# Kernel optimization log

Measured on AMD Instinct MI355X. Metric: run time of the kernel, lower is better.

## Reference

```python
import jax, jax.numpy as jnp
import numpy as np

B, T, C, H = 4, 2048, 768, 12
D = C // H  # head dim = 64

def setup_inputs() -> dict:
    key = jax.random.key(0)
    k1, k2, k3 = jax.random.split(key, 3)
    x = jax.random.normal(k1, (B, T, C), dtype=jnp.float32)
    W_attn = jax.random.normal(k2, (C, 3 * C), dtype=jnp.float32) * 0.02
    b_attn = jnp.zeros((3 * C,), dtype=jnp.float32)
    W_proj = jax.random.normal(k3, (C, C), dtype=jnp.float32) * 0.02
    b_proj = jnp.zeros((C,), dtype=jnp.float32)
    return {"x": x, "W_attn": W_attn, "b_attn": b_attn, "W_proj": W_proj, "b_proj": b_proj}

def reference(x, W_attn, b_attn, W_proj, b_proj):
    Bx, Tx, Cx = x.shape
    qkv = x @ W_attn + b_attn                      # [B,T,3C]
    q, k, v = jnp.split(qkv, 3, axis=2)
    q = q.reshape(Bx, Tx, H, D).swapaxes(1, 2)     # [B,H,T,D]
    k = k.reshape(Bx, Tx, H, D).swapaxes(1, 2)
    v = v.reshape(Bx, Tx, H, D).swapaxes(1, 2)
    att = jnp.einsum('bhqd,bhkd->bhqk', q, k) / jnp.sqrt(jnp.float32(D))
    mask = jnp.tril(jnp.ones((Tx, Tx), dtype=bool))
    att = jnp.where(mask, att, -jnp.inf)
    att = jax.nn.softmax(att, axis=-1)
    y = jnp.einsum('bhqk,bhkd->bhqd', att, v)      # [B,H,T,D]
    y = y.swapaxes(1, 2).reshape(Bx, Tx, Cx)
    return y @ W_proj + b_proj
```

## Files before the change

### kernel.cpp

```cpp
#include <hip/hip_runtime.h>
#include <hip/hip_bf16.h>

#define BATCH 4
#define TSEQ  2048
#define CDIM  768
#define HNUM  12
#define DHEAD 64
#define NQKV  (3*CDIM)
#define BTOT  (BATCH*TSEQ)
#define BH    (BATCH*HNUM)

typedef unsigned short u16;
typedef __attribute__((ext_vector_type(8))) __bf16 bf16x8;
typedef __attribute__((ext_vector_type(4))) float f32x4;

#define MFMA16(a,b,c) __builtin_amdgcn_mfma_f32_16x16x32_bf16((a),(b),(c),0,0,0)

__device__ __forceinline__ u16 f2b(float f) {
    union { float f; unsigned u; } v; v.f = f;
    unsigned u = v.u;
    unsigned r = (u + 0x7fffu + ((u >> 16) & 1u)) >> 16;
    return (u16)r;
}

__device__ __forceinline__ unsigned cvtpk(float lo, float hi) {
    unsigned r;
    asm("v_cvt_pk_bf16_f32 %0, %1, %2" : "=v"(r) : "v"(lo), "v"(hi));
    return r;
}

__device__ __forceinline__ float fexp2(float x) {
    float r;
    asm("v_exp_f32 %0, %1" : "=v"(r) : "v"(x));
    return r;
}

__device__ __forceinline__ void gload_lds(const void* g, void* l) {
    __builtin_amdgcn_global_load_lds(
        (const __attribute__((address_space(1))) void*)g,
        (__attribute__((address_space(3))) void*)l, 16, 0, 0);
}

__global__ __launch_bounds__(256) void cast_f32_bf16(
        const float* __restrict__ in, u16* __restrict__ out, int n4) {
    int i = blockIdx.x * blockDim.x + threadIdx.x;
    if (i >= n4) return;
    float4 a = reinterpret_cast<const float4*>(in)[i];
    ushort4 o;
    o.x = f2b(a.x); o.y = f2b(a.y); o.z = f2b(a.z); o.w = f2b(a.w);
    reinterpret_cast<ushort4*>(out)[i] = o;
}

__global__ __launch_bounds__(256) void tcast(
        const float* __restrict__ in, u16* __restrict__ out, int R, int Cc) {
    __shared__ float tile[32][33];
    int c0 = blockIdx.x * 32, r0 = blockIdx.y * 32;
    int tx = threadIdx.x, ty = threadIdx.y;
    #pragma unroll
    for (int i = 0; i < 32; i += 8)
        tile[ty + i][tx] = in[(size_t)(r0 + ty + i) * Cc + c0 + tx];
    __syncthreads();
    #pragma unroll
    for (int i = 0; i < 32; i += 8)
        out[(size_t)(c0 + ty + i) * R + r0 + tx] = f2b(tile[tx][ty + i]);
}

template<int NX>
__global__ __launch_bounds__(256, 2) void gemm_qkv(
        const u16* __restrict__ A, const u16* __restrict__ Bt,
        const float* __restrict__ bias,
        u16* __restrict__ qb, u16* __restrict__ kb, u16* __restrict__ vtb,
        int K) {
    __shared__ u16 sA[3][128 * 32];
    __shared__ u16 sB[3][256 * 32];
    const int tid = threadIdx.x;
    const int lane = tid & 63;
    const int w = tid >> 6;
    const int g = lane >> 4, lr = lane & 15;
    const int cpx = gridDim.x >> 3;
    const int wg = ((int)blockIdx.x & 7) * cpx + ((int)blockIdx.x >> 3);
    const int bx = wg % NX, by = wg / NX;
    const int m0 = by * 128, n0 = bx * 256;

    f32x4 acc[8][4] = {};

    auto stage = [&](int buf, int kt) {
        #pragma unroll
        for (int i = 0; i < 2; ++i) {
            int c = i * 256 + tid, r = c >> 2, s = c & 3;
            int c8 = s ^ ((r >> 1) & 3);
            gload_lds(A + (size_t)(m0 + r) * K + kt * 32 + c8 * 8, &sA[buf][c * 8]);
        }
        #pragma unroll
        for (int i = 0; i < 4; ++i) {
            int c = i * 256 + tid, r = c >> 2, s = c & 3;
            int c8 = s ^ ((r >> 1) & 3);
            gload_lds(Bt + (size_t)(n0 + r) * K + kt * 32 + c8 * 8, &sB[buf][c * 8]);
        }
    };

    const int KT = K / 32;
    stage(0, 0); stage(1, 1);
    for (int kt = 0; kt < KT; ++kt) {
        if (kt + 1 < KT) asm volatile("s_waitcnt vmcnt(6)" ::: "memory");
        else             asm volatile("s_waitcnt vmcnt(0)" ::: "memory");
        __builtin_amdgcn_s_barrier();
        if (kt + 2 < KT) stage((kt + 2) % 3, kt + 2);
        const u16* cA = sA[kt % 3];
        const u16* cB = sB[kt % 3];
        bf16x8 af[8], bfr[4];
        #pragma unroll
        for (int m = 0; m < 8; ++m) {
            int r = m * 16 + lr;
            af[m] = *(const bf16x8*)&cA[r * 32 + ((g ^ ((r >> 1) & 3)) << 3)];
        }
        #pragma unroll
        for (int n = 0; n < 4; ++n) {
            int r = w * 64 + n * 16 + lr;
            bfr[n] = *(const bf16x8*)&cB[r * 32 + ((g ^ ((r >> 1) & 3)) << 3)];
        }
        __builtin_amdgcn_s_setprio(1);
        #pragma unroll
        for (int m = 0; m < 8; ++m)
            #pragma unroll
            for (int n = 0; n < 4; ++n)
                acc[m][n] = MFMA16(bfr[n], af[m], acc[m][n]);
        __builtin_amdgcn_s_setprio(0);
    }

    const int which = n0 / CDIM;
    #pragma unroll
    for (int m = 0; m < 8; ++m) {
        const int rg = m0 + m * 16 + lr;
        const int b = rg >> 11, t = rg & (TSEQ - 1);
        #pragma unroll
        for (int n = 0; n < 4; ++n) {
            const int cg = n0 + w * 64 + n * 16 + (g << 2);
            const int c  = cg - which * CDIM;
            const int h  = c >> 6, d = c & 63;
            const size_t bh = (size_t)(b * HNUM + h);
            const float4 bv = *(const float4*)&bias[cg];
            const float v0 = acc[m][n][0] + bv.x;
            const float v1 = acc[m][n][1] + bv.y;
            const float v2 = acc[m][n][2] + bv.z;
            const float v3 = acc[m][n][3] + bv.w;
            if (which == 0) {
                const float s = 0.1803368801111243f;
                ushort4 pv;
                pv.x = f2b(v0 * s); pv.y = f2b(v1 * s);
                pv.z = f2b(v2 * s); pv.w = f2b(v3 * s);
                *(ushort4*)&qb[(bh * TSEQ + t) * DHEAD + d] = pv;
            } else if (which == 1) {
                ushort4 pv;
                pv.x = f2b(v0); pv.y = f2b(v1); pv.z = f2b(v2); pv.w = f2b(v3);
                *(ushort4*)&kb[(bh * TSEQ + t) * DHEAD + d] = pv;
            } else {
                vtb[(bh * DHEAD + d + 0) * TSEQ + t] = f2b(v0);
                vtb[(bh * DHEAD + d + 1) * TSEQ + t] = f2b(v1);
                vtb[(bh * DHEAD + d + 2) * TSEQ + t] = f2b(v2);
                vtb[(bh * DHEAD + d + 3) * TSEQ + t] = f2b(v3);
            }
        }
    }
}

template<int NX>
__global__ __launch_bounds__(256) void gemm_out(
        const u16* __restrict__ A, const u16* __restrict__ Bt,
        const float* __restrict__ bias, float* __restrict__ outf, int K) {
    __shared__ u16 sA[3][128 * 32];
    __shared__ u16 sB[3][128 * 32];
    const int tid = threadIdx.x;
    const int lane = tid & 63;
    const int w = tid >> 6;
    const int wr = w >> 1, wc = w & 1;
    const int cpx = gridDim.x >> 3;
    const int wg = ((int)blockIdx.x & 7) * cpx + ((int)blockIdx.x >> 3);
    const int bx = wg % NX, by = wg / NX;
    const int m0 = by * 128, n0 = bx * 128;

    f32x4 acc[4][4] = {};

    auto stage = [&](int buf, int kt) {
        #pragma unroll
        for (int i = 0; i < 2; ++i) {
            int chunk = i * 256 + tid;
            int row = chunk >> 2, c8 = chunk & 3;
            gload_lds(A  + (size_t)(m0 + row) * K + kt * 32 + c8 * 8, &sA[buf][chunk * 8]);
            gload_lds(Bt + (size_t)(n0 + row) * K + kt * 32 + c8 * 8, &sB[buf][chunk * 8]);
        }
    };

    const int KT = K / 32;
    stage(0, 0); stage(1, 1);
    for (int kt = 0; kt < KT; ++kt) {
        if (kt + 1 < KT) asm volatile("s_waitcnt vmcnt(4)" ::: "memory");
        else             asm volatile("s_waitcnt vmcnt(0)" ::: "memory");
        __builtin_amdgcn_s_barrier();
        if (kt + 2 < KT) stage((kt + 2) % 3, kt + 2);
        const u16* cA = sA[kt % 3];
        const u16* cB = sB[kt % 3];
        bf16x8 af[4], bfr[4];
        #pragma unroll
        for (int m = 0; m < 4; ++m)
            af[m] = *(const bf16x8*)&cA[(wr * 64 + m * 16 + (lane & 15)) * 32 + ((lane >> 4) << 3)];
        #pragma unroll
        for (int n = 0; n < 4; ++n)
            bfr[n] = *(const bf16x8*)&cB[(wc * 64 + n * 16 + (lane & 15)) * 32 + ((lane >> 4) << 3)];
        #pragma unroll
        for (int m = 0; m < 4; ++m)
            #pragma unroll
            for (int n = 0; n < 4; ++n)
                acc[m][n] = MFMA16(bfr[n], af[m], acc[m][n]);
    }

    #pragma unroll
    for (int m = 0; m < 4; ++m) {
        const int rg = m0 + wr * 64 + m * 16 + (lane & 15);
        #pragma unroll
        for (int n = 0; n < 4; ++n) {
            const int cg = n0 + wc * 64 + n * 16 + ((lane >> 4) << 2);
            const float4 bv = *(const float4*)&bias[cg];
            float4 ov;
            ov.x = acc[m][n][0] + bv.x;
            ov.y = acc[m][n][1] + bv.y;
            ov.z = acc[m][n][2] + bv.z;
            ov.w = acc[m][n][3] + bv.w;
            *(float4*)&outf[(size_t)rg * CDIM + cg] = ov;
        }
    }
}

__global__ __launch_bounds__(256, 4) void attn_fwd(
        const u16* __restrict__ qb, const u16* __restrict__ kb,
        const u16* __restrict__ vtb, u16* __restrict__ yb) {
    __shared__ u16 sK[2][64 * 64];
    __shared__ u16 sVt[2][64 * 64];
    const int qt = 31 - (int)(blockIdx.x / BH);
    const int bh = blockIdx.x % BH;
    const int b = bh / HNUM, h = bh % HNUM;
    const int tid = threadIdx.x, lane = tid & 63, w = tid >> 6;
    const int g = lane >> 4, lq = lane & 15;
    const int qlo = qt * 64 + w * 16;
    const u16* qbase = qb  + (size_t)bh * TSEQ * DHEAD;
    const u16* kbase = kb  + (size_t)bh * TSEQ * DHEAD;
    const u16* vbase = vtb + (size_t)bh * DHEAD * TSEQ;

    bf16x8 qf[2];
    #pragma unroll
    for (int ks = 0; ks < 2; ++ks)
        qf[ks] = *(const bf16x8*)&qbase[(size_t)(qlo + lq) * DHEAD + ks * 32 + g * 8];

    union { unsigned u[4]; bf16x8 v; } ones;
    #pragma unroll
    for (int i = 0; i < 4; ++i) ones.u[i] = 0x3f803f80u;

    f32x4 o[4] = {};
    f32x4 ls = {};
    float mx = -__builtin_inff();

    auto STAGE = [&](int buf, int kt) {
        const int k0 = kt << 6;
        #pragma unroll
        for (int i = 0; i < 2; ++i) {
            int chunk = i * 256 + tid;
            int srow = chunk >> 3;
            int cb = ((chunk & 7) << 4) ^ ((srow & 7) << 4);
            gload_lds(kbase + (size_t)(k0 + srow) * DHEAD + (cb >> 1), &sK[buf][chunk * 8]);
            gload_lds(vbase + (size_t)srow * TSEQ + k0 + (cb >> 1),    &sVt[buf][chunk * 8]);
        }
    };

    const int nk = qt + 1;
    STAGE(0, 0);
    __syncthreads();
    for (int kt = 0; kt < nk; ++kt) {
        const int k0 = kt << 6;
        if (kt + 1 < nk) STAGE((kt + 1) & 1, kt + 1);
        const u16* cK = sK[kt & 1];
        const u16* cV = sVt[kt & 1];
        f32x4 s[4];
        #pragma unroll
        for (int n = 0; n < 4; ++n) s[n] = f32x4{0.f, 0.f, 0.f, 0.f};
        __builtin_amdgcn_s_setprio(1);
        #pragma unroll
        for (int n = 0; n < 4; ++n) {
            #pragma unroll
            for (int ks = 0; ks < 2; ++ks) {
                int r = n * 16 + lq;
                int lb = (r * 128 + (ks * 32 + g * 8) * 2) ^ ((r & 7) << 4);
                bf16x8 kf = *(const bf16x8*)((const char*)cK + lb);
                s[n] = MFMA16(kf, qf[ks], s[n]);
            }
        }
        __builtin_amdgcn_s_setprio(0);
        if (k0 + 63 > qlo) {
            const int qa = qlo + lq;
            #pragma unroll
            for (int n = 0; n < 4; ++n)
                #pragma unroll
                for (int j = 0; j < 4; ++j)
                    if (k0 + n * 16 + g * 4 + j > qa) s[n][j] = -__builtin_inff();
        }
        float t0 = fmaxf(fmaxf(s[0][0], s[0][1]), fmaxf(s[0][2], s[0][3]));
        float t1 = fmaxf(fmaxf(s[1][0], s[1][1]), fmaxf(s[1][2], s[1][3]));
        float t2 = fmaxf(fmaxf(s[2][0], s[2][1]), fmaxf(s[2][2], s[2][3]));
        float t3 = fmaxf(fmaxf(s[3][0], s[3][1]), fmaxf(s[3][2], s[3][3]));
        float tmax = fmaxf(fmaxf(t0, t1), fmaxf(t2, t3));
        tmax = fmaxf(tmax, __shfl_xor(tmax, 16));
        tmax = fmaxf(tmax, __shfl_xor(tmax, 32));
        if (__any(tmax > mx + 8.0f)) {
            float mnew = fmaxf(mx, tmax);
            float sc = fexp2(mx - mnew);
            mx = mnew;
            #pragma unroll
            for (int j = 0; j < 4; ++j) {
                float scj = __shfl(sc, (lane & 48) | ((g << 2) + j));
                ls[j] *= scj;
                #pragma unroll
                for (int n = 0; n < 4; ++n) o[n][j] *= scj;
            }
        }
        #pragma unroll
        for (int n = 0; n < 4; ++n)
            #pragma unroll
            for (int j = 0; j < 4; ++j)
                s[n][j] = fexp2(s[n][j] - mx);
        unsigned apk[4], bpk[4];
        #pragma unroll
        for (int n = 0; n < 4; ++n) {
            apk[n] = cvtpk(s[n][0], s[n][1]);
            bpk[n] = cvtpk(s[n][2], s[n][3]);
        }
        const int s0l = lq + ((lane & 16) << 1);
        const bool hi = (lane & 32) != 0;
        #pragma unroll
        for (int ks = 0; ks < 2; ++ks) {
            unsigned A0  = (unsigned)__shfl((int)apk[2 * ks],     s0l);
            unsigned B0  = (unsigned)__shfl((int)bpk[2 * ks],     s0l);
            unsigned A1  = (unsigned)__shfl((int)apk[2 * ks + 1], s0l);
            unsigned B1  = (unsigned)__shfl((int)bpk[2 * ks + 1], s0l);
            unsigned A0h = (unsigned)__shfl((int)apk[2 * ks],     s0l + 16);
            unsigned B0h = (unsigned)__shfl((int)bpk[2 * ks],     s0l + 16);
            unsigned A1h = (unsigned)__shfl((int)apk[2 * ks + 1], s0l + 16);
            unsigned B1h = (unsigned)__shfl((int)bpk[2 * ks + 1], s0l + 16);
            union { unsigned u[4]; bf16x8 v; } pa;
            pa.u[0] = hi ? A1  : A0;
            pa.u[1] = hi ? B1  : B0;
            pa.u[2] = hi ? A1h : A0h;
            pa.u[3] = hi ? B1h : B0h;
            __builtin_amdgcn_s_setprio(1);
            #pragma unroll
            for (int n = 0; n < 4; ++n) {
                int d = n * 16 + lq;
                int lb = (d * 128 + (ks * 32 + g * 8) * 2) ^ ((d & 7) << 4);
                bf16x8 vf = *(const bf16x8*)((const char*)cV + lb);
                o[n] = MFMA16(pa.v, vf, o[n]);
            }
            ls = MFMA16(pa.v, ones.v, ls);
            __builtin_amdgcn_s_setprio(0);
        }
        __syncthreads();
    }

    #pragma unroll
    for (int j = 0; j < 4; ++j) {
        float inv = 1.f / ls[j];
        const int t = qlo + g * 4 + j;
        #pragma unroll
        for (int n = 0; n < 4; ++n) {
            const int c = h * DHEAD + n * 16 + lq;
            yb[((size_t)b * TSEQ + t) * CDIM + c] = f2b(o[n][j] * inv);
        }
    }
}

extern "C" void kernel_launch(void* const* d_in, const int* in_sizes, int n_in,
                              void* d_out, int out_size, void* d_ws, size_t ws_size,
                              hipStream_t stream) {
    const float* x      = (const float*)d_in[0];
    const float* W_attn = (const float*)d_in[1];
    const float* b_attn = (const float*)d_in[2];
    const float* W_proj = (const float*)d_in[3];
    const float* b_proj = (const float*)d_in[4];
    float* out = (float*)d_out;

    u16* ws = (u16*)d_ws;
    u16* xb     = ws;
    u16* yb     = xb;
    u16* WattnT = xb     + (size_t)BTOT * CDIM;
    u16* WprojT = WattnT + (size_t)NQKV * CDIM;
    u16* qb     = WprojT + (size_t)CDIM * CDIM;
    u16* kb     = qb     + (size_t)BH * TSEQ * DHEAD;
    u16* vtb    = kb     + (size_t)BH * TSEQ * DHEAD;

    int n4 = BTOT * CDIM / 4;
    cast_f32_bf16<<<(n4 + 255) / 256, 256, 0, stream>>>(x, xb, n4);
    tcast<<<dim3(NQKV / 32, CDIM / 32), dim3(32, 8), 0, stream>>>(W_attn, WattnT, CDIM, NQKV);
    tcast<<<dim3(CDIM / 32, CDIM / 32), dim3(32, 8), 0, stream>>>(W_proj, WprojT, CDIM, CDIM);

    gemm_qkv<NQKV / 256><<<dim3((NQKV / 256) * (BTOT / 128)), 256, 0, stream>>>(
        xb, WattnT, b_attn, qb, kb, vtb, CDIM);

    attn_fwd<<<dim3((TSEQ / 64) * BH), 256, 0, stream>>>(qb, kb, vtb, yb);

    gemm_out<CDIM / 128><<<dim3((CDIM / 128) * (BTOT / 128)), 256, 0, stream>>>(
        yb, WprojT, b_proj, out, CDIM);
}
```

Measured before the change: 152.3 us.

## Fuse x fp32-to-bf16 cast into QKV GEMM and merge weight transposes

Removes the separate cast kernel for x. The QKV GEMM now loads fp32 activations directly into LDS and converts them to bf16 in registers before the MFMA. The two weight transpose-cast launches are merged into a single kernel. The GEMM tile shrinks from 128x256 to 128x128 with a 2x2 wave layout, and the 3-stage pipeline with explicit vmcnt waits is replaced by double buffering with full __syncthreads. In exchange, the A-side LDS traffic doubles (fp32 instead of bf16), x is re-read in fp32 by every column tile, and the simpler pipeline may expose more load latency.

```diff
diff --git a/kernel.cpp b/kernel.cpp
--- a/kernel.cpp
+++ b/kernel.cpp
@@ -41,20 +41,14 @@
         (__attribute__((address_space(3))) void*)l, 16, 0, 0);
 }
 
-__global__ __launch_bounds__(256) void cast_f32_bf16(
-        const float* __restrict__ in, u16* __restrict__ out, int n4) {
-    int i = blockIdx.x * blockDim.x + threadIdx.x;
-    if (i >= n4) return;
-    float4 a = reinterpret_cast<const float4*>(in)[i];
-    ushort4 o;
-    o.x = f2b(a.x); o.y = f2b(a.y); o.z = f2b(a.z); o.w = f2b(a.w);
-    reinterpret_cast<ushort4*>(out)[i] = o;
-}
-
-__global__ __launch_bounds__(256) void tcast(
-        const float* __restrict__ in, u16* __restrict__ out, int R, int Cc) {
+__global__ __launch_bounds__(256) void tcast2(
+        const float* __restrict__ Wa, const float* __restrict__ Wp,
+        u16* __restrict__ WaT, u16* __restrict__ WpT) {
     __shared__ float tile[32][33];
-    int c0 = blockIdx.x * 32, r0 = blockIdx.y * 32;
+    const float* in; u16* out; int Cc; int bx = blockIdx.x;
+    if (bx < NQKV / 32) { in = Wa; out = WaT; Cc = NQKV; }
+    else                { in = Wp; out = WpT; Cc = CDIM; bx -= NQKV / 32; }
+    int c0 = bx * 32, r0 = blockIdx.y * 32;
     int tx = threadIdx.x, ty = threadIdx.y;
     #pragma unroll
     for (int i = 0; i < 32; i += 8)
@@ -62,80 +56,86 @@
     __syncthreads();
     #pragma unroll
     for (int i = 0; i < 32; i += 8)
-        out[(size_t)(c0 + ty + i) * R + r0 + tx] = f2b(tile[tx][ty + i]);
+        out[(size_t)(c0 + ty + i) * CDIM + r0 + tx] = f2b(tile[tx][ty + i]);
 }
 
 template<int NX>
-__global__ __launch_bounds__(256, 2) void gemm_qkv(
-        const u16* __restrict__ A, const u16* __restrict__ Bt,
+__global__ __launch_bounds__(256) void gemm_qkv(
+        const float* __restrict__ X, const u16* __restrict__ Bt,
         const float* __restrict__ bias,
         u16* __restrict__ qb, u16* __restrict__ kb, u16* __restrict__ vtb,
         int K) {
-    __shared__ u16 sA[3][128 * 32];
-    __shared__ u16 sB[3][256 * 32];
+    __shared__ float sA[2][128 * 32];
+    __shared__ u16   sB[2][128 * 32];
     const int tid = threadIdx.x;
     const int lane = tid & 63;
     const int w = tid >> 6;
-    const int g = lane >> 4, lr = lane & 15;
+    const int wr = w >> 1, wc = w & 1;
+    const int g = lane >> 4;
     const int cpx = gridDim.x >> 3;
     const int wg = ((int)blockIdx.x & 7) * cpx + ((int)blockIdx.x >> 3);
     const int bx = wg % NX, by = wg / NX;
-    const int m0 = by * 128, n0 = bx * 256;
-
-    f32x4 acc[8][4] = {};
+    const int m0 = by * 128, n0 = bx * 128;
+
+    f32x4 acc[4][4] = {};
 
     auto stage = [&](int buf, int kt) {
         #pragma unroll
+        for (int i = 0; i < 4; ++i) {
+            int c = i * 256 + tid;
+            int r = c >> 3, p = c & 7;
+            int l = p ^ (r & 7);
+            gload_lds(X + (size_t)(m0 + r) * K + kt * 32 + l * 4, &sA[buf][c * 4]);
+        }
+        #pragma unroll
         for (int i = 0; i < 2; ++i) {
-            int c = i * 256 + tid, r = c >> 2, s = c & 3;
-            int c8 = s ^ ((r >> 1) & 3);
-            gload_lds(A + (size_t)(m0 + r) * K + kt * 32 + c8 * 8, &sA[buf][c * 8]);
-        }
-        #pragma unroll
-        for (int i = 0; i < 4; ++i) {
-            int c = i * 256 + tid, r = c >> 2, s = c & 3;
-            int c8 = s ^ ((r >> 1) & 3);
-            gload_lds(Bt + (size_t)(n0 + r) * K + kt * 32 + c8 * 8, &sB[buf][c * 8]);
+            int c = i * 256 + tid;
+            int row = c >> 2, c8 = c & 3;
+            gload_lds(Bt + (size_t)(n0 + row) * K + kt * 32 + c8 * 8, &sB[buf][c * 8]);
         }
     };
 
     const int KT = K / 32;
-    stage(0, 0); stage(1, 1);
+    stage(0, 0);
+    __syncthreads();
     for (int kt = 0; kt < KT; ++kt) {
-        if (kt + 1 < KT) asm volatile("s_waitcnt vmcnt(6)" ::: "memory");
-        else             asm volatile("s_waitcnt vmcnt(0)" ::: "memory");
-        __builtin_amdgcn_s_barrier();
-        if (kt + 2 < KT) stage((kt + 2) % 3, kt + 2);
-        const u16* cA = sA[kt % 3];
-        const u16* cB = sB[kt % 3];
-        bf16x8 af[8], bfr[4];
-        #pragma unroll
-        for (int m = 0; m < 8; ++m) {
-            int r = m * 16 + lr;
-            af[m] = *(const bf16x8*)&cA[r * 32 + ((g ^ ((r >> 1) & 3)) << 3)];
-        }
-        #pragma unroll
-        for (int n = 0; n < 4; ++n) {
-            int r = w * 64 + n * 16 + lr;
-            bfr[n] = *(const bf16x8*)&cB[r * 32 + ((g ^ ((r >> 1) & 3)) << 3)];
-        }
+        if (kt + 1 < KT) stage((kt + 1) & 1, kt + 1);
+        const float* cA = sA[kt & 1];
+        const u16*  cB = sB[kt & 1];
+        bf16x8 af[4], bfr[4];
+        #pragma unroll
+        for (int m = 0; m < 4; ++m) {
+            int r = wr * 64 + m * 16 + (lane & 15);
+            float4 a0 = *(const float4*)&cA[r * 32 + (((2 * g)     ^ (r & 7)) << 2)];
+            float4 a1 = *(const float4*)&cA[r * 32 + (((2 * g + 1) ^ (r & 7)) << 2)];
+            union { unsigned u[4]; bf16x8 v; } t;
+            t.u[0] = cvtpk(a0.x, a0.y);
+            t.u[1] = cvtpk(a0.z, a0.w);
+            t.u[2] = cvtpk(a1.x, a1.y);
+            t.u[3] = cvtpk(a1.z, a1.w);
+            af[m] = t.v;
+        }
+        #pragma unroll
+        for (int n = 0; n < 4; ++n)
+            bfr[n] = *(const bf16x8*)&cB[(wc * 64 + n * 16 + (lane & 15)) * 32 + (g << 3)];
         __builtin_amdgcn_s_setprio(1);
         #pragma unroll
-        for (int m = 0; m < 8; ++m)
+        for (int m = 0; m < 4; ++m)
             #pragma unroll
             for (int n = 0; n < 4; ++n)
                 acc[m][n] = MFMA16(bfr[n], af[m], acc[m][n]);
         __builtin_amdgcn_s_setprio(0);
+        __syncthreads();
     }
 
     const int which = n0 / CDIM;
     #pragma unroll
-    for (int m = 0; m < 8; ++m) {
-        const int rg = m0 + m * 16 + lr;
+    for (int m = 0; m < 4; ++m) {
+        const int rg = m0 + wr * 64 + m * 16 + (lane & 15);
         const int b = rg >> 11, t = rg & (TSEQ - 1);
         #pragma unroll
         for (int n = 0; n < 4; ++n) {
-            const int cg = n0 + w * 64 + n * 16 + (g << 2);
+            const int cg = n0 + wc * 64 + n * 16 + (g << 2);
             const int c  = cg - which * CDIM;
             const int h  = c >> 6, d = c & 63;
             const size_t bh = (size_t)(b * HNUM + h);
@@ -386,21 +386,18 @@
     float* out = (float*)d_out;
 
     u16* ws = (u16*)d_ws;
-    u16* xb     = ws;
-    u16* yb     = xb;
-    u16* WattnT = xb     + (size_t)BTOT * CDIM;
+    u16* yb     = ws;
+    u16* WattnT = yb     + (size_t)BTOT * CDIM;
     u16* WprojT = WattnT + (size_t)NQKV * CDIM;
     u16* qb     = WprojT + (size_t)CDIM * CDIM;
     u16* kb     = qb     + (size_t)BH * TSEQ * DHEAD;
     u16* vtb    = kb     + (size_t)BH * TSEQ * DHEAD;
 
-    int n4 = BTOT * CDIM / 4;
-    cast_f32_bf16<<<(n4 + 255) / 256, 256, 0, stream>>>(x, xb, n4);
-    tcast<<<dim3(NQKV / 32, CDIM / 32), dim3(32, 8), 0, stream>>>(W_attn, WattnT, CDIM, NQKV);
-    tcast<<<dim3(CDIM / 32, CDIM / 32), dim3(32, 8), 0, stream>>>(W_proj, WprojT, CDIM, CDIM);
-
-    gemm_qkv<NQKV / 256><<<dim3((NQKV / 256) * (BTOT / 128)), 256, 0, stream>>>(
-        xb, WattnT, b_attn, qb, kb, vtb, CDIM);
+    tcast2<<<dim3(NQKV / 32 + CDIM / 32, CDIM / 32), dim3(32, 8), 0, stream>>>(
+        W_attn, W_proj, WattnT, WprojT);
+
+    gemm_qkv<NQKV / 128><<<dim3((NQKV / 128) * (BTOT / 128)), 256, 0, stream>>>(
+        x, WattnT, b_attn, qb, kb, vtb, CDIM);
 
     attn_fwd<<<dim3((TSEQ / 64) * BH), 256, 0, stream>>>(qb, kb, vtb, yb);
 
```

Measured after the change: 142.5 us. 6.5% less time.
